# Optimization experiments

Hardware: AMD Instinct MI355X
Metric: run time of the kernel (lower is better)

The kernel has to match this reference:

```python
import jax, jax.numpy as jnp
import numpy as np

B_, T_, D_ = 2, 2048, 1024
DS_, EXPAND_ = 16, 2
DI_ = D_ * EXPAND_


def setup_inputs() -> dict:
    key = jax.random.key(0)
    ks = jax.random.split(key, 10)
    s = 0.02
    x = jax.random.normal(ks[0], (B_, T_, D_), jnp.float32)
    Win = jax.random.normal(ks[1], (2 * DI_, D_), jnp.float32) * s   # in_proj weight [2di, d]
    A_log = jax.random.uniform(ks[2], (DI_, DS_), jnp.float32, -4.0, -1.0)
    WB = jax.random.normal(ks[3], (DS_, D_), jnp.float32) * s        # B_proj
    WC = jax.random.normal(ks[4], (DS_, D_), jnp.float32) * s        # C_proj
    Wdt = jax.random.normal(ks[5], (DI_, D_), jnp.float32) * s       # dt_proj weight
    bdt = jnp.zeros((DI_,), jnp.float32)                              # dt_proj bias
    dt_bias = jnp.full((DI_,), -4.0, jnp.float32)
    gamma = jnp.ones((DI_,), jnp.float32)
    beta = jnp.zeros((DI_,), jnp.float32)
    Wout = jax.random.normal(ks[6], (D_, DI_), jnp.float32) * s      # out_proj
    return dict(x=x, Win=Win, A_log=A_log, WB=WB, WC=WC, Wdt=Wdt, bdt=bdt,
                dt_bias=dt_bias, gamma=gamma, beta=beta, Wout=Wout)


def _forward(x, Win, A_log, WB, WC, Wdt, bdt, dt_bias, gamma, beta, Wout):
    B, T, d = x.shape
    di, ds = A_log.shape
    xz = jnp.einsum('btd,ed->bte', x, Win)            # [B,T,2di]
    xi, z = xz[..., :di], xz[..., di:]
    z = jax.nn.silu(z)
    A = -jnp.exp(A_log)                                # [di,ds]
    Bm = jnp.einsum('btd,sd->bts', x, WB)              # [B,T,ds]
    C = jnp.einsum('btd,sd->bts', x, WC)               # [B,T,ds]
    dt = jax.nn.softplus(jnp.einsum('btd,ed->bte', x, Wdt) + bdt + dt_bias)  # [B,T,di]
    dtA = dt[..., None] * A                            # [B,T,di,ds]
    denom = 1.0 - dtA * 0.5
    A_bar = (1.0 + dtA * 0.5) / denom                  # bilinear (Tustin)
    B_bar = dt[..., None] / denom                      # [B,T,di,ds]

    def step(state, inp):
        Ab, Bb, Bt, xt, Ct = inp                       # [B,di,ds],[B,di,ds],[B,ds],[B,di],[B,ds]
        state = Ab * state + Bb * Bt[:, None, :] * xt[:, :, None]
        out = jnp.einsum('bds,bs->bd', state, Ct)
        return state, out

    tm = lambda a: jnp.swapaxes(a, 0, 1)               # time-major for scan
    state0 = jnp.zeros((B, di, ds), x.dtype)
    state, outs = jax.lax.scan(step, state0, (tm(A_bar), tm(B_bar), tm(Bm), tm(xi), tm(C)))
    out = jnp.swapaxes(outs, 0, 1) * z                 # [B,T,di]
    mu = out.mean(-1, keepdims=True)
    var = ((out - mu) ** 2).mean(-1, keepdims=True)
    normed = (out - mu) * jax.lax.rsqrt(var + 1e-5) * gamma + beta
    y = jnp.einsum('bte,de->btd', normed, Wout)
    return y, state


def reference(x, Win, A_log, WB, WC, Wdt, bdt, dt_bias, gamma, beta, Wout):
    return _forward(x, Win, A_log, WB, WC, Wdt, bdt, dt_bias, gamma, beta, Wout)
```

## Files before the change

kernel.cpp:

```cpp
#include <hip/hip_runtime.h>
#include <stdint.h>

#define B_ 2
#define T_ 2048
#define D_ 1024
#define DI_ 2048
#define DS_ 16
#define MROWS (B_*T_)
#define NC_ 32
#define CL_ (T_/NC_)
#define TT_ 32

typedef unsigned short u16;
typedef __attribute__((ext_vector_type(4))) float f32x4;
typedef __attribute__((ext_vector_type(8))) short short8;
typedef __attribute__((ext_vector_type(4))) unsigned short u16x4;

__device__ __forceinline__ float bf2f(u16 u) {
    union { uint32_t i; float f; } v; v.i = ((uint32_t)u) << 16; return v.f;
}
__device__ __forceinline__ u16 f2bf(float f) {
    union { float f; uint32_t i; } v; v.f = f;
    uint32_t r = v.i + 0x7fff + ((v.i >> 16) & 1);
    return (u16)(r >> 16);
}

__global__ __launch_bounds__(256) void cvt_kernel(const float* __restrict__ in,
                                                  u16* __restrict__ out, int n4) {
    int i = blockIdx.x * 256 + threadIdx.x;
    if (i < n4) {
        float4 v = ((const float4*)in)[i];
        u16x4 o;
        o.x = f2bf(v.x); o.y = f2bf(v.y); o.z = f2bf(v.z); o.w = f2bf(v.w);
        ((u16x4*)out)[i] = o;
    }
}

__global__ __launch_bounds__(256) void gemm_in(
    const u16* __restrict__ A, const u16* __restrict__ Win,
    const u16* __restrict__ Wdt,
    u16* __restrict__ xi, u16* __restrict__ z, u16* __restrict__ dtout,
    const float* __restrict__ b1, const float* __restrict__ b2) {
    __shared__ u16 lA[128 * 32];
    __shared__ u16 lB[128 * 32];
    const int K = D_;
    const int tid  = threadIdx.x;
    const int lane = tid & 63;
    const int wave = tid >> 6;
    const int wr = wave >> 1, wc = wave & 1;
    const int m0 = blockIdx.y * 128, n0 = blockIdx.x * 128;
    const int region = n0 >> 11;
    const u16* W = (region < 2) ? (Win + (size_t)n0 * K)
                                : (Wdt + (size_t)(n0 - 4096) * K);

    f32x4 acc[4][4];
#pragma unroll
    for (int i = 0; i < 4; ++i)
#pragma unroll
        for (int j = 0; j < 4; ++j) acc[i][j] = (f32x4){0.f, 0.f, 0.f, 0.f};

    const int lrow = tid >> 2;
    const int lseg = tid & 3;

    for (int k0 = 0; k0 < K; k0 += 32) {
        __syncthreads();
#pragma unroll
        for (int it = 0; it < 2; ++it) {
            int row = it * 64 + lrow;
            const u16* sa = A + (size_t)(m0 + row) * K + k0 + lseg * 8;
            const u16* sw = W + (size_t)row * K + k0 + lseg * 8;
            __builtin_amdgcn_global_load_lds(
                (const __attribute__((address_space(1))) void*)sa,
                (__attribute__((address_space(3))) void*)(lA + row * 32 + lseg * 8),
                16, 0, 0);
            __builtin_amdgcn_global_load_lds(
                (const __attribute__((address_space(1))) void*)sw,
                (__attribute__((address_space(3))) void*)(lB + row * 32 + lseg * 8),
                16, 0, 0);
        }
        __syncthreads();

        const int fr = lane & 15, ks = lane >> 4;
        short8 af[4], bfr[4];
#pragma unroll
        for (int i = 0; i < 4; ++i) {
            af[i]  = *(const short8*)(lA + (wr * 64 + i * 16 + fr) * 32 + ks * 8);
            bfr[i] = *(const short8*)(lB + (wc * 64 + i * 16 + fr) * 32 + ks * 8);
        }
#pragma unroll
        for (int i = 0; i < 4; ++i)
#pragma unroll
            for (int j = 0; j < 4; ++j)
                acc[i][j] = __builtin_amdgcn_mfma_f32_16x16x32_bf16(
                    af[i], bfr[j], acc[i][j], 0, 0, 0);
    }

    const int fr = lane & 15, fq = lane >> 4;
#pragma unroll
    for (int i = 0; i < 4; ++i)
#pragma unroll
        for (int j = 0; j < 4; ++j) {
            int gnl = n0 + wc * 64 + j * 16 + fr;
#pragma unroll
            for (int r = 0; r < 4; ++r) {
                int gm = m0 + wr * 64 + i * 16 + fq * 4 + r;
                float v = acc[i][j][r];
                if (region == 0) {
                    xi[(size_t)gm * DI_ + gnl] = f2bf(v);
                } else if (region == 1) {
                    v = v / (1.f + __expf(-v));
                    z[(size_t)gm * DI_ + (gnl - 2048)] = f2bf(v);
                } else {
                    int gn = gnl - 4096;
                    v += b1[gn] + b2[gn];
                    v = (v > 20.f) ? v : log1pf(__expf(v));
                    dtout[(size_t)gm * DI_ + gn] = f2bf(v);
                }
            }
        }
}

__global__ __launch_bounds__(256) void gemm_out(
    const u16* __restrict__ A, const u16* __restrict__ W,
    float* __restrict__ out, int M, int N, int K) {
    __shared__ u16 lA[128 * 32];
    __shared__ u16 lB[128 * 32];
    const int tid  = threadIdx.x;
    const int lane = tid & 63;
    const int wave = tid >> 6;
    const int wr = wave >> 1, wc = wave & 1;
    const int m0 = blockIdx.y * 128, n0 = blockIdx.x * 128;

    f32x4 acc[4][4];
#pragma unroll
    for (int i = 0; i < 4; ++i)
#pragma unroll
        for (int j = 0; j < 4; ++j) acc[i][j] = (f32x4){0.f, 0.f, 0.f, 0.f};

    const int lrow = tid >> 2;
    const int lseg = tid & 3;

    for (int k0 = 0; k0 < K; k0 += 32) {
        __syncthreads();
#pragma unroll
        for (int it = 0; it < 2; ++it) {
            int row = it * 64 + lrow;
            const u16* sa = A + (size_t)(m0 + row) * K + k0 + lseg * 8;
            const u16* sw = W + (size_t)(n0 + row) * K + k0 + lseg * 8;
            __builtin_amdgcn_global_load_lds(
                (const __attribute__((address_space(1))) void*)sa,
                (__attribute__((address_space(3))) void*)(lA + row * 32 + lseg * 8),
                16, 0, 0);
            __builtin_amdgcn_global_load_lds(
                (const __attribute__((address_space(1))) void*)sw,
                (__attribute__((address_space(3))) void*)(lB + row * 32 + lseg * 8),
                16, 0, 0);
        }
        __syncthreads();

        const int fr = lane & 15, ks = lane >> 4;
        short8 af[4], bfr[4];
#pragma unroll
        for (int i = 0; i < 4; ++i) {
            af[i]  = *(const short8*)(lA + (wr * 64 + i * 16 + fr) * 32 + ks * 8);
            bfr[i] = *(const short8*)(lB + (wc * 64 + i * 16 + fr) * 32 + ks * 8);
        }
#pragma unroll
        for (int i = 0; i < 4; ++i)
#pragma unroll
            for (int j = 0; j < 4; ++j)
                acc[i][j] = __builtin_amdgcn_mfma_f32_16x16x32_bf16(
                    af[i], bfr[j], acc[i][j], 0, 0, 0);
    }

    const int fr = lane & 15, fq = lane >> 4;
#pragma unroll
    for (int i = 0; i < 4; ++i)
#pragma unroll
        for (int j = 0; j < 4; ++j) {
            int gn = n0 + wc * 64 + j * 16 + fr;
#pragma unroll
            for (int r = 0; r < 4; ++r) {
                int gm = m0 + wr * 64 + i * 16 + fq * 4 + r;
                out[(size_t)gm * N + gn] = acc[i][j][r];
            }
        }
}

__global__ __launch_bounds__(256) void bc_kernel(
    const float* __restrict__ x, const float* __restrict__ WB,
    const float* __restrict__ WC, float* __restrict__ Bm, float* __restrict__ Cm) {
    __shared__ float xs[32][65];
    __shared__ float ws[32][65];
    int m0 = blockIdx.x * 32;
    int tid = threadIdx.x;
    int o = tid & 31, mg = tid >> 5;
    float acc[4] = {0.f, 0.f, 0.f, 0.f};
    for (int k0 = 0; k0 < D_; k0 += 64) {
        __syncthreads();
#pragma unroll
        for (int j = 0; j < 8; ++j) {
            int f = j * 256 + tid;
            int r = f >> 6, kk = f & 63;
            xs[r][kk] = x[(size_t)(m0 + r) * D_ + k0 + kk];
            ws[r][kk] = (r < 16) ? WB[(size_t)r * D_ + k0 + kk]
                                 : WC[(size_t)(r - 16) * D_ + k0 + kk];
        }
        __syncthreads();
#pragma unroll 8
        for (int kk = 0; kk < 64; ++kk) {
            float wv = ws[o][kk];
#pragma unroll
            for (int r = 0; r < 4; ++r)
                acc[r] = fmaf(xs[mg * 4 + r][kk], wv, acc[r]);
        }
    }
#pragma unroll
    for (int r = 0; r < 4; ++r) {
        int m = m0 + mg * 4 + r;
        if (o < 16) Bm[(size_t)m * DS_ + o] = acc[r];
        else        Cm[(size_t)m * DS_ + (o - 16)] = acc[r];
    }
}


__global__ __launch_bounds__(256) void scan1_kernel(
    const u16* __restrict__ dt, const u16* __restrict__ xi,
    const float* __restrict__ Bm, const float* __restrict__ A_log,
    float* __restrict__ P, float* __restrict__ Z) {
    const int c = blockIdx.x, dblk = blockIdx.y, b = blockIdx.z;
    const int tid = threadIdx.x;
    const int d = dblk * 256 + tid;
    __shared__ u16 sdt[TT_ * 256];
    __shared__ u16 sxi[TT_ * 256];
    __shared__ float sB[TT_ * 16];
    float A2[16], st[16], Pp[16];
#pragma unroll
    for (int s = 0; s < 16; ++s) {
        A2[s] = -0.5f * __expf(A_log[(size_t)d * DS_ + s]);
        st[s] = 0.f; Pp[s] = 1.f;
    }
    const size_t tb = (size_t)b * T_;
    for (int t0 = c * CL_; t0 < (c + 1) * CL_; t0 += TT_) {
        __syncthreads();
#pragma unroll
        for (int r = 0; r < 4; ++r) {
            int flat = r * 2048 + tid * 8;
            int row = flat >> 8, col = flat & 255;
            const u16* s1 = dt + (tb + t0 + row) * DI_ + dblk * 256 + col;
            const u16* s2 = xi + (tb + t0 + row) * DI_ + dblk * 256 + col;
            __builtin_amdgcn_global_load_lds(
                (const __attribute__((address_space(1))) void*)s1,
                (__attribute__((address_space(3))) void*)(sdt + flat), 16, 0, 0);
            __builtin_amdgcn_global_load_lds(
                (const __attribute__((address_space(1))) void*)s2,
                (__attribute__((address_space(3))) void*)(sxi + flat), 16, 0, 0);
        }
        *(float2*)(sB + tid * 2) = *(const float2*)(Bm + (tb + t0) * DS_ + tid * 2);
        __syncthreads();
#pragma unroll 2
        for (int tt = 0; tt < TT_; ++tt) {
            float dtv = bf2f(sdt[tt * 256 + tid]);
            float xiv = bf2f(sxi[tt * 256 + tid]);
            float dxv = dtv * xiv;
            float bv[16];
            *(float4*)&bv[0]  = *(const float4*)(sB + tt * 16);
            *(float4*)&bv[4]  = *(const float4*)(sB + tt * 16 + 4);
            *(float4*)&bv[8]  = *(const float4*)(sB + tt * 16 + 8);
            *(float4*)&bv[12] = *(const float4*)(sB + tt * 16 + 12);
#pragma unroll
            for (int s = 0; s < 16; ++s) {
                float a2   = fmaf(dtv, -A2[s], 1.f);
                float inv  = __builtin_amdgcn_rcpf(a2);
                float abar = fmaf(2.f, inv, -1.f);
                st[s] = fmaf(abar, st[s], (inv * bv[s]) * dxv);
                Pp[s] *= abar;
            }
        }
    }
    size_t base = (((size_t)b * DI_ + d) * NC_ + c) * 16;
#pragma unroll
    for (int q = 0; q < 4; ++q) {
        *(float4*)(P + base + q * 4) = (float4){Pp[q*4], Pp[q*4+1], Pp[q*4+2], Pp[q*4+3]};
        *(float4*)(Z + base + q * 4) = (float4){st[q*4], st[q*4+1], st[q*4+2], st[q*4+3]};
    }
}

__global__ __launch_bounds__(256) void scan2_kernel(
    float* __restrict__ P, const float* __restrict__ Z,
    float* __restrict__ st_out) {
    size_t idx = (size_t)blockIdx.x * 256 + threadIdx.x;
    size_t bd = idx >> 4;
    int s = (int)(idx & 15);
    float cur = 0.f;
    for (int c = 0; c < NC_; ++c) {
        size_t a = (bd * NC_ + c) * 16 + s;
        float p = P[a], zv = Z[a];
        P[a] = cur;
        cur = fmaf(p, cur, zv);
    }
    st_out[idx] = cur;
}

__global__ __launch_bounds__(256) void scan3_kernel(
    const u16* __restrict__ dt, const u16* __restrict__ xi,
    const float* __restrict__ Bm, const float* __restrict__ Cm,
    const float* __restrict__ A_log, const float* __restrict__ I,
    u16* __restrict__ so) {
    const int c = blockIdx.x, dblk = blockIdx.y, b = blockIdx.z;
    const int tid = threadIdx.x;
    const int d = dblk * 256 + tid;
    __shared__ u16 sdt[TT_ * 256];
    __shared__ u16 sxi[TT_ * 256];
    __shared__ float sB[TT_ * 16];
    __shared__ float sC[TT_ * 16];
    float A2[16], st[16];
#pragma unroll
    for (int s = 0; s < 16; ++s)
        A2[s] = -0.5f * __expf(A_log[(size_t)d * DS_ + s]);
    size_t base = (((size_t)b * DI_ + d) * NC_ + c) * 16;
#pragma unroll
    for (int q = 0; q < 4; ++q) {
        float4 v = *(const float4*)(I + base + q * 4);
        st[q*4] = v.x; st[q*4+1] = v.y; st[q*4+2] = v.z; st[q*4+3] = v.w;
    }
    const size_t tb = (size_t)b * T_;
    for (int t0 = c * CL_; t0 < (c + 1) * CL_; t0 += TT_) {
        __syncthreads();
#pragma unroll
        for (int r = 0; r < 4; ++r) {
            int flat = r * 2048 + tid * 8;
            int row = flat >> 8, col = flat & 255;
            const u16* s1 = dt + (tb + t0 + row) * DI_ + dblk * 256 + col;
            const u16* s2 = xi + (tb + t0 + row) * DI_ + dblk * 256 + col;
            __builtin_amdgcn_global_load_lds(
                (const __attribute__((address_space(1))) void*)s1,
                (__attribute__((address_space(3))) void*)(sdt + flat), 16, 0, 0);
            __builtin_amdgcn_global_load_lds(
                (const __attribute__((address_space(1))) void*)s2,
                (__attribute__((address_space(3))) void*)(sxi + flat), 16, 0, 0);
        }
        *(float2*)(sB + tid * 2) = *(const float2*)(Bm + (tb + t0) * DS_ + tid * 2);
        *(float2*)(sC + tid * 2) = *(const float2*)(Cm + (tb + t0) * DS_ + tid * 2);
        __syncthreads();
#pragma unroll 2
        for (int tt = 0; tt < TT_; ++tt) {
            float dtv = bf2f(sdt[tt * 256 + tid]);
            float xiv = bf2f(sxi[tt * 256 + tid]);
            float dxv = dtv * xiv;
            float bv[16], cv[16];
            *(float4*)&bv[0]  = *(const float4*)(sB + tt * 16);
            *(float4*)&bv[4]  = *(const float4*)(sB + tt * 16 + 4);
            *(float4*)&bv[8]  = *(const float4*)(sB + tt * 16 + 8);
            *(float4*)&bv[12] = *(const float4*)(sB + tt * 16 + 12);
            *(float4*)&cv[0]  = *(const float4*)(sC + tt * 16);
            *(float4*)&cv[4]  = *(const float4*)(sC + tt * 16 + 4);
            *(float4*)&cv[8]  = *(const float4*)(sC + tt * 16 + 8);
            *(float4*)&cv[12] = *(const float4*)(sC + tt * 16 + 12);
            float acc = 0.f;
#pragma unroll
            for (int s = 0; s < 16; ++s) {
                float a2   = fmaf(dtv, -A2[s], 1.f);
                float inv  = __builtin_amdgcn_rcpf(a2);
                float abar = fmaf(2.f, inv, -1.f);
                st[s] = fmaf(abar, st[s], (inv * bv[s]) * dxv);
                acc = fmaf(st[s], cv[s], acc);
            }
            so[(tb + t0 + tt) * DI_ + d] = f2bf(acc);
        }
    }
}

__global__ __launch_bounds__(256) void ln_kernel(
    const u16* __restrict__ so, const u16* __restrict__ z,
    const float* __restrict__ gamma, const float* __restrict__ beta,
    u16* __restrict__ normed) {
    int m = blockIdx.x;
    int tid = threadIdx.x;
    size_t base = (size_t)m * DI_;
    float v[8];
    float s = 0.f, s2 = 0.f;
#pragma unroll
    for (int j = 0; j < 8; ++j) {
        int i = tid + j * 256;
        float val = bf2f(so[base + i]) * bf2f(z[base + i]);
        v[j] = val; s += val; s2 += val * val;
    }
#pragma unroll
    for (int off = 32; off; off >>= 1) {
        s  += __shfl_xor(s,  off);
        s2 += __shfl_xor(s2, off);
    }
    __shared__ float rs[4], rq[4];
    int wave = tid >> 6;
    if ((tid & 63) == 0) { rs[wave] = s; rq[wave] = s2; }
    __syncthreads();
    s  = rs[0] + rs[1] + rs[2] + rs[3];
    s2 = rq[0] + rq[1] + rq[2] + rq[3];
    float mu  = s * (1.f / DI_);
    float var = s2 * (1.f / DI_) - mu * mu;
    float rstd = rsqrtf(var + 1e-5f);
#pragma unroll
    for (int j = 0; j < 8; ++j) {
        int i = tid + j * 256;
        float nv = (v[j] - mu) * rstd * gamma[i] + beta[i];
        normed[base + i] = f2bf(nv);
    }
}

extern "C" void kernel_launch(void* const* d_in, const int* in_sizes, int n_in,
                              void* d_out, int out_size, void* d_ws, size_t ws_size,
                              hipStream_t stream) {
    const float* x       = (const float*)d_in[0];
    const float* Win     = (const float*)d_in[1];
    const float* A_log   = (const float*)d_in[2];
    const float* WB      = (const float*)d_in[3];
    const float* WC      = (const float*)d_in[4];
    const float* Wdt     = (const float*)d_in[5];
    const float* bdt     = (const float*)d_in[6];
    const float* dt_bias = (const float*)d_in[7];
    const float* gamma   = (const float*)d_in[8];
    const float* beta    = (const float*)d_in[9];
    const float* Wout    = (const float*)d_in[10];

    float* y_out     = (float*)d_out;
    float* state_out = y_out + (size_t)B_ * T_ * D_;

    char* ws = (char*)d_ws;
    u16* xi_bf   = (u16*)(ws + 0);
    u16* z_bf    = (u16*)(ws + 16777216);
    u16* dt_bf   = (u16*)(ws + 33554432);
    u16* so_bf   = (u16*)(ws + 50331648);
    u16* nm_bf   = (u16*)(ws + 67108864);
    u16* x_bf    = (u16*)(ws + 83886080);
    u16* win_bf  = (u16*)(ws + 92274688);
    u16* wdt_bf  = (u16*)(ws + 100663296);
    u16* wout_bf = (u16*)(ws + 104857600);
    float* BmB   = (float*)(ws + 109051904);
    float* CmB   = (float*)(ws + 109314048);

    float* Pc = (float*)(ws + 83886080);
    float* Zc = (float*)(ws + 92274688);

    {
        int n4;
        n4 = (B_ * T_ * D_) / 4;
        cvt_kernel<<<(n4 + 255) / 256, 256, 0, stream>>>(x, x_bf, n4);
        n4 = (2 * DI_ * D_) / 4;
        cvt_kernel<<<(n4 + 255) / 256, 256, 0, stream>>>(Win, win_bf, n4);
        n4 = (DI_ * D_) / 4;
        cvt_kernel<<<(n4 + 255) / 256, 256, 0, stream>>>(Wdt, wdt_bf, n4);
        n4 = (D_ * DI_) / 4;
        cvt_kernel<<<(n4 + 255) / 256, 256, 0, stream>>>(Wout, wout_bf, n4);
    }

    dim3 blk(256);
    gemm_in<<<dim3(6144 / 128, MROWS / 128), blk, 0, stream>>>(
        x_bf, win_bf, wdt_bf, xi_bf, z_bf, dt_bf, bdt, dt_bias);
    bc_kernel<<<MROWS / 32, 256, 0, stream>>>(x, WB, WC, BmB, CmB);

    scan1_kernel<<<dim3(NC_, DI_ / 256, B_), blk, 0, stream>>>(
        dt_bf, xi_bf, BmB, A_log, Pc, Zc);
    scan2_kernel<<<(B_ * DI_ * DS_) / 256, blk, 0, stream>>>(
        Pc, Zc, state_out);
    scan3_kernel<<<dim3(NC_, DI_ / 256, B_), blk, 0, stream>>>(
        dt_bf, xi_bf, BmB, CmB, A_log, Pc, so_bf);

    ln_kernel<<<MROWS, 256, 0, stream>>>(so_bf, z_bf, gamma, beta, nm_bf);
    gemm_out<<<dim3(D_ / 128, MROWS / 128), blk, 0, stream>>>(
        nm_bf, wout_bf, y_out, MROWS, D_, DI_);
}
```

Before: 443.1 us.

## Double-buffer GEMM LDS tiles, XOR-swizzle LDS layout, and remap workgroups

After: 415.6 us. 1.07x faster.

```diff
diff --git a/kernel.cpp b/kernel.cpp
--- a/kernel.cpp
+++ b/kernel.cpp
@@ -41,14 +41,19 @@
     const u16* __restrict__ Wdt,
     u16* __restrict__ xi, u16* __restrict__ z, u16* __restrict__ dtout,
     const float* __restrict__ b1, const float* __restrict__ b2) {
-    __shared__ u16 lA[128 * 32];
-    __shared__ u16 lB[128 * 32];
+    __shared__ u16 lA[2][128 * 32];
+    __shared__ u16 lB[2][128 * 32];
     const int K = D_;
     const int tid  = threadIdx.x;
     const int lane = tid & 63;
     const int wave = tid >> 6;
     const int wr = wave >> 1, wc = wave & 1;
-    const int m0 = blockIdx.y * 128, n0 = blockIdx.x * 128;
+
+    const int nwg = gridDim.x * gridDim.y;
+    const int lin = blockIdx.y * gridDim.x + blockIdx.x;
+    const int swz = (lin & 7) * (nwg >> 3) + (lin >> 3);
+    const int bx = swz % gridDim.x, by = swz / gridDim.x;
+    const int m0 = by * 128, n0 = bx * 128;
     const int region = n0 >> 11;
     const u16* W = (region < 2) ? (Win + (size_t)n0 * K)
                                 : (Wdt + (size_t)(n0 - 4096) * K);
@@ -59,33 +64,40 @@
 #pragma unroll
         for (int j = 0; j < 4; ++j) acc[i][j] = (f32x4){0.f, 0.f, 0.f, 0.f};
 
-    const int lrow = tid >> 2;
-    const int lseg = tid & 3;
-
+    const int srow = tid >> 2;
+    const int sseg = tid & 3;
+    const int gseg = sseg ^ ((srow >> 1) & 3);
+
+    const int fr = lane & 15, ks = lane >> 4;
+    const int rsw = ks ^ ((fr >> 1) & 3);
+
+    auto STAGE = [&](int buf, int k0) {
+#pragma unroll
+        for (int it = 0; it < 2; ++it) {
+            int row = it * 64 + srow;
+            const u16* sa = A + (size_t)(m0 + row) * K + k0 + gseg * 8;
+            const u16* sw = W + (size_t)row * K + k0 + gseg * 8;
+            __builtin_amdgcn_global_load_lds(
+                (const __attribute__((address_space(1))) void*)sa,
+                (__attribute__((address_space(3))) void*)(&lA[buf][row * 32 + sseg * 8]),
+                16, 0, 0);
+            __builtin_amdgcn_global_load_lds(
+                (const __attribute__((address_space(1))) void*)sw,
+                (__attribute__((address_space(3))) void*)(&lB[buf][row * 32 + sseg * 8]),
+                16, 0, 0);
+        }
+    };
+
+    STAGE(0, 0);
+    __syncthreads();
+    int cur = 0;
     for (int k0 = 0; k0 < K; k0 += 32) {
-        __syncthreads();
-#pragma unroll
-        for (int it = 0; it < 2; ++it) {
-            int row = it * 64 + lrow;
-            const u16* sa = A + (size_t)(m0 + row) * K + k0 + lseg * 8;
-            const u16* sw = W + (size_t)row * K + k0 + lseg * 8;
-            __builtin_amdgcn_global_load_lds(
-                (const __attribute__((address_space(1))) void*)sa,
-                (__attribute__((address_space(3))) void*)(lA + row * 32 + lseg * 8),
-                16, 0, 0);
-            __builtin_amdgcn_global_load_lds(
-                (const __attribute__((address_space(1))) void*)sw,
-                (__attribute__((address_space(3))) void*)(lB + row * 32 + lseg * 8),
-                16, 0, 0);
-        }
-        __syncthreads();
-
-        const int fr = lane & 15, ks = lane >> 4;
+        if (k0 + 32 < K) STAGE(cur ^ 1, k0 + 32);
         short8 af[4], bfr[4];
 #pragma unroll
         for (int i = 0; i < 4; ++i) {
-            af[i]  = *(const short8*)(lA + (wr * 64 + i * 16 + fr) * 32 + ks * 8);
-            bfr[i] = *(const short8*)(lB + (wc * 64 + i * 16 + fr) * 32 + ks * 8);
+            af[i]  = *(const short8*)(&lA[cur][(wr * 64 + i * 16 + fr) * 32 + rsw * 8]);
+            bfr[i] = *(const short8*)(&lB[cur][(wc * 64 + i * 16 + fr) * 32 + rsw * 8]);
         }
 #pragma unroll
         for (int i = 0; i < 4; ++i)
@@ -93,9 +105,11 @@
             for (int j = 0; j < 4; ++j)
                 acc[i][j] = __builtin_amdgcn_mfma_f32_16x16x32_bf16(
                     af[i], bfr[j], acc[i][j], 0, 0, 0);
-    }
-
-    const int fr = lane & 15, fq = lane >> 4;
+        __syncthreads();
+        cur ^= 1;
+    }
+
+    const int fq = lane >> 4;
 #pragma unroll
     for (int i = 0; i < 4; ++i)
 #pragma unroll
@@ -123,13 +137,18 @@
 __global__ __launch_bounds__(256) void gemm_out(
     const u16* __restrict__ A, const u16* __restrict__ W,
     float* __restrict__ out, int M, int N, int K) {
-    __shared__ u16 lA[128 * 32];
-    __shared__ u16 lB[128 * 32];
+    __shared__ u16 lA[2][128 * 32];
+    __shared__ u16 lB[2][128 * 32];
     const int tid  = threadIdx.x;
     const int lane = tid & 63;
     const int wave = tid >> 6;
     const int wr = wave >> 1, wc = wave & 1;
-    const int m0 = blockIdx.y * 128, n0 = blockIdx.x * 128;
+
+    const int nwg = gridDim.x * gridDim.y;
+    const int lin = blockIdx.y * gridDim.x + blockIdx.x;
+    const int swz = (lin & 7) * (nwg >> 3) + (lin >> 3);
+    const int bx = swz % gridDim.x, by = swz / gridDim.x;
+    const int m0 = by * 128, n0 = bx * 128;
 
     f32x4 acc[4][4];
 #pragma unroll
@@ -137,33 +156,39 @@
 #pragma unroll
         for (int j = 0; j < 4; ++j) acc[i][j] = (f32x4){0.f, 0.f, 0.f, 0.f};
 
-    const int lrow = tid >> 2;
-    const int lseg = tid & 3;
-
+    const int srow = tid >> 2;
+    const int sseg = tid & 3;
+    const int gseg = sseg ^ ((srow >> 1) & 3);
+    const int fr = lane & 15, ks = lane >> 4;
+    const int rsw = ks ^ ((fr >> 1) & 3);
+
+    auto STAGE = [&](int buf, int k0) {
+#pragma unroll
+        for (int it = 0; it < 2; ++it) {
+            int row = it * 64 + srow;
+            const u16* sa = A + (size_t)(m0 + row) * K + k0 + gseg * 8;
+            const u16* sw = W + (size_t)(n0 + row) * K + k0 + gseg * 8;
+            __builtin_amdgcn_global_load_lds(
+                (const __attribute__((address_space(1))) void*)sa,
+                (__attribute__((address_space(3))) void*)(&lA[buf][row * 32 + sseg * 8]),
+                16, 0, 0);
+            __builtin_amdgcn_global_load_lds(
+                (const __attribute__((address_space(1))) void*)sw,
+                (__attribute__((address_space(3))) void*)(&lB[buf][row * 32 + sseg * 8]),
+                16, 0, 0);
+        }
+    };
+
+    STAGE(0, 0);
+    __syncthreads();
+    int cur = 0;
     for (int k0 = 0; k0 < K; k0 += 32) {
-        __syncthreads();
-#pragma unroll
-        for (int it = 0; it < 2; ++it) {
-            int row = it * 64 + lrow;
-            const u16* sa = A + (size_t)(m0 + row) * K + k0 + lseg * 8;
-            const u16* sw = W + (size_t)(n0 + row) * K + k0 + lseg * 8;
-            __builtin_amdgcn_global_load_lds(
-                (const __attribute__((address_space(1))) void*)sa,
-                (__attribute__((address_space(3))) void*)(lA + row * 32 + lseg * 8),
-                16, 0, 0);
-            __builtin_amdgcn_global_load_lds(
-                (const __attribute__((address_space(1))) void*)sw,
-                (__attribute__((address_space(3))) void*)(lB + row * 32 + lseg * 8),
-                16, 0, 0);
-        }
-        __syncthreads();
-
-        const int fr = lane & 15, ks = lane >> 4;
+        if (k0 + 32 < K) STAGE(cur ^ 1, k0 + 32);
         short8 af[4], bfr[4];
 #pragma unroll
         for (int i = 0; i < 4; ++i) {
-            af[i]  = *(const short8*)(lA + (wr * 64 + i * 16 + fr) * 32 + ks * 8);
-            bfr[i] = *(const short8*)(lB + (wc * 64 + i * 16 + fr) * 32 + ks * 8);
+            af[i]  = *(const short8*)(&lA[cur][(wr * 64 + i * 16 + fr) * 32 + rsw * 8]);
+            bfr[i] = *(const short8*)(&lB[cur][(wc * 64 + i * 16 + fr) * 32 + rsw * 8]);
         }
 #pragma unroll
         for (int i = 0; i < 4; ++i)
@@ -171,9 +196,11 @@
             for (int j = 0; j < 4; ++j)
                 acc[i][j] = __builtin_amdgcn_mfma_f32_16x16x32_bf16(
                     af[i], bfr[j], acc[i][j], 0, 0, 0);
-    }
-
-    const int fr = lane & 15, fq = lane >> 4;
+        __syncthreads();
+        cur ^= 1;
+    }
+
+    const int fq = lane >> 4;
 #pragma unroll
     for (int i = 0; i < 4; ++i)
 #pragma unroll
@@ -222,7 +249,6 @@
         else        Cm[(size_t)m * DS_ + (o - 16)] = acc[r];
     }
 }
-
 
 __global__ __launch_bounds__(256) void scan1_kernel(
     const u16* __restrict__ dt, const u16* __restrict__ xi,
```
